# Optimization experiments

Hardware: AMD Instinct MI355X
Metric: run time of the kernel (lower is better)

The kernel has to match this reference:

```python
import jax, jax.numpy as jnp
import numpy as np

B, S, H = 32, 256, 1024   # batch, seq_len, xlmr hidden
HL = 512                  # lstm hidden per direction
E = 256                   # entity_feature_size
L = 5                     # languages: en fr de es it
LN_EPS = 1e-5


def setup_inputs() -> dict:
    key = jax.random.key(0)
    ks = jax.random.split(key, 12)
    sc = 0.02
    sequence_output = jax.random.normal(ks[0], (B, S, H), jnp.float32)
    lengths = jax.random.randint(ks[1], (B,), S // 2, S + 1)
    attention_mask = (jnp.arange(S)[None, :] < lengths[:, None]).astype(jnp.int32)
    language_ids = jax.random.randint(ks[2], (B,), 0, L).astype(jnp.int64)
    # per-language adapter params (stacked over lang dim)
    W1 = jax.random.normal(ks[3], (L, H, H), jnp.float32) * sc
    b1 = jnp.zeros((L, H), jnp.float32)
    ln_g = jnp.ones((L, H), jnp.float32)
    ln_b = jnp.zeros((L, H), jnp.float32)
    W2 = jax.random.normal(ks[4], (L, H, H), jnp.float32) * sc
    b2 = jnp.zeros((L, H), jnp.float32)
    # BiLSTM params, torch gate order (i, f, g, o); b = b_ih + b_hh
    Wih_f = jax.random.normal(ks[5], (4 * HL, H), jnp.float32) * sc
    Whh_f = jax.random.normal(ks[6], (4 * HL, HL), jnp.float32) * sc
    b_f = jnp.zeros((4 * HL,), jnp.float32)
    Wih_b = jax.random.normal(ks[7], (4 * HL, H), jnp.float32) * sc
    Whh_b = jax.random.normal(ks[8], (4 * HL, HL), jnp.float32) * sc
    b_b = jnp.zeros((4 * HL,), jnp.float32)
    # projection 2*HL -> E
    Wp = jax.random.normal(ks[9], (E, 2 * HL), jnp.float32) * sc
    bp = jnp.zeros((E,), jnp.float32)
    return dict(sequence_output=sequence_output, attention_mask=attention_mask,
                language_ids=language_ids, W1=W1, b1=b1, ln_g=ln_g, ln_b=ln_b,
                W2=W2, b2=b2, Wih_f=Wih_f, Whh_f=Whh_f, b_f=b_f,
                Wih_b=Wih_b, Whh_b=Whh_b, b_b=b_b, Wp=Wp, bp=bp)


def _lstm_scan(x, mask, Wih, Whh, b):
    """x: [S,B,H], mask: [S,B,1] bool. Returns hidden states [S,B,HL].
    Masked steps keep state and emit 0 (pack/pad_packed semantics)."""
    h0 = jnp.zeros((x.shape[1], Whh.shape[1]), x.dtype)

    def step(carry, inp):
        h, c = carry
        x_t, m = inp
        gates = x_t @ Wih.T + h @ Whh.T + b
        i, f, g, o = jnp.split(gates, 4, axis=-1)
        c_new = jax.nn.sigmoid(f) * c + jax.nn.sigmoid(i) * jnp.tanh(g)
        h_new = jax.nn.sigmoid(o) * jnp.tanh(c_new)
        h = jnp.where(m, h_new, h)
        c = jnp.where(m, c_new, c)
        return (h, c), jnp.where(m, h_new, 0.0)

    _, ys = jax.lax.scan(step, (h0, h0), (x, mask))
    return ys


def reference(sequence_output, attention_mask, language_ids, W1, b1, ln_g, ln_b,
              W2, b2, Wih_f, Whh_f, b_f, Wih_b, Whh_b, b_b, Wp, bp):
    # --- all 5 language adapters on the full batch, then masked-sum ---
    h = jnp.einsum('bsh,lhd->lbsd', sequence_output, W1) + b1[:, None, None, :]
    mu = h.mean(-1, keepdims=True)
    var = h.var(-1, keepdims=True)
    h = (h - mu) * jax.lax.rsqrt(var + LN_EPS) * ln_g[:, None, None, :] + ln_b[:, None, None, :]
    h = jax.nn.relu(h)
    h = jnp.einsum('lbsd,ldh->lbsh', h, W2) + b2[:, None, None, :]
    onehot = jax.nn.one_hot(language_ids, L, dtype=h.dtype)          # [B,L]
    adapted = jnp.einsum('lbsh,bl->bsh', h, onehot)                  # [B,S,H]
    # --- BiLSTM over valid lengths (packed-sequence semantics) ---
    x = adapted.transpose(1, 0, 2)                                    # [S,B,H]
    m = attention_mask.astype(bool).T[:, :, None]                     # [S,B,1]
    ys_f = _lstm_scan(x, m, Wih_f, Whh_f, b_f)                        # [S,B,HL]
    ys_b = _lstm_scan(x[::-1], m[::-1], Wih_b, Whh_b, b_b)[::-1]      # [S,B,HL]
    lstm_out = jnp.concatenate([ys_f, ys_b], -1).transpose(1, 0, 2)   # [B,S,2HL]
    return lstm_out @ Wp.T + bp                                       # [B,S,E]
```

## Files before the change

### kernel.cpp

```cpp
#include <hip/hip_runtime.h>

typedef __bf16 bft;
typedef bft bf16x8 __attribute__((ext_vector_type(8)));
typedef bft bf16x4 __attribute__((ext_vector_type(4)));
typedef bft bf16x2 __attribute__((ext_vector_type(2)));
typedef float f32x4 __attribute__((ext_vector_type(4)));
typedef unsigned long long u64;
typedef unsigned int u32;
typedef u32 u32x4 __attribute__((ext_vector_type(4)));

#define LN_EPS 1e-5f


__device__ __forceinline__ float sigmoidf_(float x) {
    return 1.f / (1.f + __expf(-x));
}
__device__ __forceinline__ float tanhf_(float x) {
    float e = __expf(-2.f * fabsf(x));
    float t = (1.f - e) / (1.f + e);
    return copysignf(t, x);
}

__global__ void cvt_f32_bf16(const float* __restrict__ in, bft* __restrict__ out, int n4) {
    int i = blockIdx.x * blockDim.x + threadIdx.x;
    if (i < n4) {
        float4 v = ((const float4*)in)[i];
        bf16x4 o = { (bft)v.x, (bft)v.y, (bft)v.z, (bft)v.w };
        ((bf16x4*)out)[i] = o;
    }
}

__global__ void zero_u32(u32* __restrict__ p, int n) {
    int i = blockIdx.x * blockDim.x + threadIdx.x;
    if (i < n) p[i] = 0u;
}

__global__ __launch_bounds__(256) void cvt_permute_wih(
    const float* __restrict__ in, bft* __restrict__ out)
{
    int r = blockIdx.x;
    int src = (r & 3) * 512 + (r >> 2);
    int t = threadIdx.x;
    float4 v = ((const float4*)(in + (size_t)src * 1024))[t];
    bf16x4 o = { (bft)v.x, (bft)v.y, (bft)v.z, (bft)v.w };
    ((bf16x4*)(out + (size_t)r * 1024))[t] = o;
}

__global__ void permute_bias(const float* __restrict__ in, float* __restrict__ out) {
    int t = blockIdx.x * blockDim.x + threadIdx.x;
    if (t < 2048) out[t] = in[(t & 3) * 512 + (t >> 2)];
}

__global__ __launch_bounds__(256) void transpose_cvt_w(
    const float* __restrict__ W1, const float* __restrict__ W2,
    bft* __restrict__ W1t, bft* __restrict__ W2t)
{
    __shared__ float tile[32][33];
    int z = blockIdx.z;
    int l = z >> 1;
    const float* src = ((z & 1) ? W2 : W1) + ((size_t)l << 20);
    bft* dst = ((z & 1) ? W2t : W1t) + ((size_t)l << 20);
    int tx = threadIdx.x & 31, ty = threadIdx.x >> 5;
    int bx = blockIdx.x * 32, by = blockIdx.y * 32;
    for (int r = ty; r < 32; r += 8)
        tile[r][tx] = src[(size_t)(by + r) * 1024 + bx + tx];
    __syncthreads();
    for (int r = ty; r < 32; r += 8)
        dst[(size_t)(bx + r) * 1024 + by + tx] = (bft)tile[tx][r];
}

__global__ __launch_bounds__(256) void gemm_bt(
    const bft* __restrict__ A, const bft* __restrict__ Bt,
    const float* __restrict__ bias, const int* __restrict__ langs,
    int langStrideB, int langStrideBias,
    float* __restrict__ outF, bft* __restrict__ outB,
    int remapLog, int remapMul, int ldc)
{
    const int K = 1024;
    int tn = blockIdx.x, tm = blockIdx.y;
    int row0 = tm * 128, col0 = tn * 128;
    int lang = langs ? langs[row0 >> 8] : 0;
    const bft* Ap = A + (size_t)row0 * K;
    const bft* Bp = Bt + (size_t)lang * langStrideB + (size_t)col0 * K;
    const float* biasp = bias + (size_t)lang * langStrideBias + col0;

    __shared__ bft As[128 * 32];
    __shared__ bft Bs[128 * 32];

    int t = threadIdx.x;
    int lane = t & 63, wave = t >> 6;
    int wm = wave & 1, wn = wave >> 1;
    int lrow = lane & 15, quad = lane >> 4;

    f32x4 acc[4][4] = {};

    for (int k0 = 0; k0 < K; k0 += 32) {
        __syncthreads();
        for (int c = t; c < 512; c += 256) {
            int r = c >> 2, co = (c & 3) << 3;
            *(uint4*)(As + r * 32 + co) = *(const uint4*)(Ap + (size_t)r * K + k0 + co);
            *(uint4*)(Bs + r * 32 + co) = *(const uint4*)(Bp + (size_t)r * K + k0 + co);
        }
        __syncthreads();
        bf16x8 af[4], bfr[4];
#pragma unroll
        for (int i = 0; i < 4; ++i)
            af[i] = *(const bf16x8*)(As + (wm * 64 + i * 16 + lrow) * 32 + quad * 8);
#pragma unroll
        for (int j = 0; j < 4; ++j)
            bfr[j] = *(const bf16x8*)(Bs + (wn * 64 + j * 16 + lrow) * 32 + quad * 8);
#pragma unroll
        for (int i = 0; i < 4; ++i)
#pragma unroll
            for (int j = 0; j < 4; ++j)
                acc[i][j] = __builtin_amdgcn_mfma_f32_16x16x32_bf16(af[i], bfr[j], acc[i][j], 0, 0, 0);
    }

#pragma unroll
    for (int i = 0; i < 4; ++i) {
#pragma unroll
        for (int j = 0; j < 4; ++j) {
#pragma unroll
            for (int r = 0; r < 4; ++r) {
                int m = wm * 64 + i * 16 + quad * 4 + r;
                int n = wn * 64 + j * 16 + lrow;
                int grow = row0 + m;
                int orow = remapLog ? ((grow & ((1 << remapLog) - 1)) * remapMul + (grow >> remapLog))
                                    : grow;
                float v = acc[i][j][r] + biasp[n];
                size_t idx = (size_t)orow * ldc + col0 + n;
                if (outF) outF[idx] = v;
                else outB[idx] = (bft)v;
            }
        }
    }
}

__global__ __launch_bounds__(256) void ln_relu_kernel(
    const float* __restrict__ h1, bft* __restrict__ a2,
    const float* __restrict__ ln_g, const float* __restrict__ ln_b,
    const int* __restrict__ langs)
{
    int row = blockIdx.x;
    int lang = langs[row >> 8];
    const float* x = h1 + (size_t)row * 1024;
    int t = threadIdx.x;
    float4 v = ((const float4*)x)[t];
    float s = v.x + v.y + v.z + v.w;
    float ss = v.x * v.x + v.y * v.y + v.z * v.z + v.w * v.w;
#pragma unroll
    for (int off = 32; off > 0; off >>= 1) {
        s += __shfl_down(s, off, 64);
        ss += __shfl_down(ss, off, 64);
    }
    __shared__ float red[8];
    int wave = t >> 6, lane = t & 63;
    if (lane == 0) { red[wave] = s; red[4 + wave] = ss; }
    __syncthreads();
    float S = red[0] + red[1] + red[2] + red[3];
    float SS = red[4] + red[5] + red[6] + red[7];
    float mean = S * (1.f / 1024.f);
    float var = SS * (1.f / 1024.f) - mean * mean;
    float inv = rsqrtf(var + LN_EPS);
    float4 g = ((const float4*)(ln_g + (size_t)lang * 1024))[t];
    float4 b = ((const float4*)(ln_b + (size_t)lang * 1024))[t];
    float y0 = fmaxf(0.f, (v.x - mean) * inv * g.x + b.x);
    float y1 = fmaxf(0.f, (v.y - mean) * inv * g.y + b.y);
    float y2 = fmaxf(0.f, (v.z - mean) * inv * g.z + b.z);
    float y3 = fmaxf(0.f, (v.w - mean) * inv * g.w + b.w);
    bf16x4 o = { (bft)y0, (bft)y1, (bft)y2, (bft)y3 };
    ((bf16x4*)(a2 + (size_t)row * 1024))[t] = o;
}

__global__ __launch_bounds__(256) void bilstm_kernel(
    const bft* __restrict__ gin_f, const bft* __restrict__ gin_b,
    const bft* __restrict__ Whh_f, const bft* __restrict__ Whh_b,
    const int* __restrict__ mask, bft* __restrict__ ys,
    u32* __restrict__ hg, u32* __restrict__ flg)
{
    __shared__ u64 smem[4096];
    bft* hs  = (bft*)smem;
    u32* hsd = (u32*)smem;

    int blk = blockIdx.x;
    int dir = blk >> 6;
    int gslice = blk & 63;
    int jbase = gslice << 3;
    const bft* Whh = dir ? Whh_b : Whh_f;
    const bft* gin = dir ? gin_b : gin_f;

    int t = threadIdx.x;
    int lane = t & 63, wave = t >> 6;
    int wm = wave & 1, wn = wave >> 1;
    int lrow = lane & 15, quad = lane >> 4;

    bf16x8 wf[16];
    {
        int row32 = wm * 16 + lrow;
        int jl = row32 >> 2, g = row32 & 3;
        const bft* wp = Whh + (size_t)(g * 512 + jbase + jl) * 512 + quad * 8;
#pragma unroll
        for (int kk = 0; kk < 16; ++kk)
            wf[kk] = *(const bf16x8*)(wp + kk * 32);
    }

    int batch = wn * 16 + lrow;
    int jl_out = wm * 4 + quad;
    const int* mrow = mask + batch * 256;
    u32* ysU = (u32*)ys;
    int mloS = t >> 6, b16S = t & 63;

    float cs = 0.f, hp = 0.f;

    for (int it = 0; it < 256; ++it) {
        int tt = dir ? (255 - it) : it;

        bf16x4 gv = *(const bf16x4*)(gin + ((size_t)(tt * 32 + batch) * 2048
                                            + (size_t)(jbase + jl_out) * 4));
        int mk = mrow[tt];

        if (it == 0) {
#pragma unroll
            for (int i = 0; i < 16; ++i)
                smem[t + i * 256] = 0ull;
        } else {
            if (wave == 0) {
                const u32* fp = flg + dir * 64 + lane;
                for (;;) {
                    u32 f = __hip_atomic_load(fp, __ATOMIC_RELAXED, __HIP_MEMORY_SCOPE_AGENT);
                    if (__all(f >= (u32)it)) break;
                    __builtin_amdgcn_s_sleep(1);
                }
            }
            __syncthreads();
            const u32* hq = hg + (size_t)(dir * 2 + (it & 1)) * 8192;
            u32x4 r[8];
#pragma unroll
            for (int i = 0; i < 8; ++i)
                asm volatile("global_load_dwordx4 %0, %1, off sc0 sc1"
                             : "=v"(r[i]) : "v"(hq + i * 1024 + t * 4) : "memory");
            asm volatile("s_waitcnt vmcnt(0)" ::: "memory");
#pragma unroll
            for (int i = 0; i < 8; ++i) {
                int m = i * 4 + mloS;
                *(u32x4*)(hsd + m * 256 + ((b16S ^ (m & 7)) << 2)) = r[i];
            }
        }
        __syncthreads();

        f32x4 acc0 = {}, acc1 = {};
#pragma unroll
        for (int kk = 0; kk < 16; ++kk) {
            int b16 = kk * 4 + quad;
            bf16x8 b = *(const bf16x8*)(hs + batch * 512 + ((b16 ^ (batch & 7)) << 3));
            if (kk & 1) acc1 = __builtin_amdgcn_mfma_f32_16x16x32_bf16(wf[kk], b, acc1, 0, 0, 0);
            else        acc0 = __builtin_amdgcn_mfma_f32_16x16x32_bf16(wf[kk], b, acc0, 0, 0, 0);
        }
        f32x4 acc = acc0 + acc1;

        float xi = acc[0] + (float)gv[0];
        float xf = acc[1] + (float)gv[1];
        float xg = acc[2] + (float)gv[2];
        float xo = acc[3] + (float)gv[3];
        float cn = sigmoidf_(xf) * cs + sigmoidf_(xi) * tanhf_(xg);
        float hn = sigmoidf_(xo) * tanhf_(cn);
        if (mk) { cs = cn; hp = hn; }
        union { bft h; unsigned short u; } hc; hc.h = (bft)hp;
        u32 own = (u32)hc.u | ((mk ? (u32)hc.u : 0u) << 16);
        u32 par = __shfl_xor(own, 16, 64);
        u32 hpair = (own & 0xffffu) | (par << 16);
        u32 ypair = (own >> 16) | (par & 0xffff0000u);

        if (!(lane & 16)) {
            u32* ha = hg + (size_t)(dir * 2 + ((it + 1) & 1)) * 8192
                         + batch * 256 + (jbase >> 1) + wm * 2 + (quad >> 1);
            asm volatile("global_store_dword %0, %1, off sc0 sc1" :: "v"(ha), "v"(hpair) : "memory");
        }
        asm volatile("s_waitcnt vmcnt(0)" ::: "memory");
        __syncthreads();
        if (t == 0 && it < 255)
            __hip_atomic_store(flg + dir * 64 + gslice, (u32)(it + 1),
                               __ATOMIC_RELAXED, __HIP_MEMORY_SCOPE_AGENT);
        if (!(lane & 16))
            ysU[((size_t)tt * 32 + batch) * 512 + dir * 256
                + (jbase >> 1) + wm * 2 + (quad >> 1)] = ypair;
    }
}

extern "C" void kernel_launch(void* const* d_in, const int* in_sizes, int n_in,
                              void* d_out, int out_size, void* d_ws, size_t ws_size,
                              hipStream_t stream)
{
    const float* X     = (const float*)d_in[0];
    const int*   amask = (const int*)d_in[1];
    const int*   langs = (const int*)d_in[2];
    const float* W1    = (const float*)d_in[3];
    const float* b1    = (const float*)d_in[4];
    const float* ln_g  = (const float*)d_in[5];
    const float* ln_b  = (const float*)d_in[6];
    const float* W2    = (const float*)d_in[7];
    const float* b2    = (const float*)d_in[8];
    const float* Wih_f = (const float*)d_in[9];
    const float* Whh_f = (const float*)d_in[10];
    const float* b_f   = (const float*)d_in[11];
    const float* Wih_b = (const float*)d_in[12];
    const float* Whh_b = (const float*)d_in[13];
    const float* b_b   = (const float*)d_in[14];
    const float* Wp    = (const float*)d_in[15];
    const float* bp    = (const float*)d_in[16];
    float* out = (float*)d_out;

    char* ws = (char*)d_ws;
    size_t off = 0;
    auto alloc = [&](size_t bytes) -> void* {
        void* p = ws + off;
        off += (bytes + 255) & ~(size_t)255;
        return p;
    };
    bft* Xbf   = (bft*)alloc(8192ull * 1024 * 2);
    bft* W1t   = (bft*)alloc(5ull * 1024 * 1024 * 2);
    bft* W2t   = (bft*)alloc(5ull * 1024 * 1024 * 2);
    bft* Wihf  = (bft*)alloc(2048ull * 1024 * 2);
    bft* Wihb  = (bft*)alloc(2048ull * 1024 * 2);
    bft* Whhf  = (bft*)alloc(2048ull * 512 * 2);
    bft* Whhb  = (bft*)alloc(2048ull * 512 * 2);
    bft* Wpb   = (bft*)alloc(256ull * 1024 * 2);
    float* h1  = (float*)alloc(8192ull * 1024 * 4);
    bft* a2    = (bft*)alloc(8192ull * 1024 * 2);
    bft* adapt = (bft*)alloc(8192ull * 1024 * 2);
    bft* ginf  = (bft*)alloc(256ull * 32 * 2048 * 2);
    bft* ginb  = (bft*)alloc(256ull * 32 * 2048 * 2);
    bft* ysb   = (bft*)alloc(256ull * 32 * 1024 * 2);
    float* pbf = (float*)alloc(2048ull * 4);
    float* pbb = (float*)alloc(2048ull * 4);
    u32* hg    = (u32*)alloc(2ull * 2 * 32 * 256 * 4);
    u32* flg   = (u32*)alloc(2ull * 64 * 4);
    (void)ws_size; (void)in_sizes; (void)n_in; (void)out_size;

    auto cvt = [&](const float* src, bft* dst, int n) {
        int n4 = n >> 2;
        hipLaunchKernelGGL(cvt_f32_bf16, dim3((n4 + 255) / 256), dim3(256), 0, stream, src, dst, n4);
    };
    cvt(X, Xbf, 8192 * 1024);
    hipLaunchKernelGGL(cvt_permute_wih, dim3(2048), dim3(256), 0, stream, Wih_f, Wihf);
    hipLaunchKernelGGL(cvt_permute_wih, dim3(2048), dim3(256), 0, stream, Wih_b, Wihb);
    cvt(Whh_f, Whhf, 2048 * 512);
    cvt(Whh_b, Whhb, 2048 * 512);
    cvt(Wp, Wpb, 256 * 1024);
    hipLaunchKernelGGL(permute_bias, dim3(8), dim3(256), 0, stream, b_f, pbf);
    hipLaunchKernelGGL(permute_bias, dim3(8), dim3(256), 0, stream, b_b, pbb);
    hipLaunchKernelGGL(zero_u32, dim3(1), dim3(256), 0, stream, flg, 128);
    hipLaunchKernelGGL(transpose_cvt_w, dim3(32, 32, 10), dim3(256), 0, stream, W1, W2, W1t, W2t);

    hipLaunchKernelGGL(gemm_bt, dim3(8, 64), dim3(256), 0, stream,
        Xbf, W1t, b1, langs, 1024 * 1024, 1024, h1, (bft*)nullptr, 0, 0, 1024);
    hipLaunchKernelGGL(ln_relu_kernel, dim3(8192), dim3(256), 0, stream, h1, a2, ln_g, ln_b, langs);
    hipLaunchKernelGGL(gemm_bt, dim3(8, 64), dim3(256), 0, stream,
        a2, W2t, b2, langs, 1024 * 1024, 1024, (float*)nullptr, adapt, 0, 0, 1024);
    hipLaunchKernelGGL(gemm_bt, dim3(16, 64), dim3(256), 0, stream,
        adapt, Wihf, pbf, (const int*)nullptr, 0, 0, (float*)nullptr, ginf, 8, 32, 2048);
    hipLaunchKernelGGL(gemm_bt, dim3(16, 64), dim3(256), 0, stream,
        adapt, Wihb, pbb, (const int*)nullptr, 0, 0, (float*)nullptr, ginb, 8, 32, 2048);
    {
        void* args[] = { (void*)&ginf, (void*)&ginb, (void*)&Whhf, (void*)&Whhb,
                         (void*)&amask, (void*)&ysb, (void*)&hg, (void*)&flg };
        hipLaunchCooperativeKernel((const void*)bilstm_kernel, dim3(128), dim3(256), args, 0, stream);
    }
    hipLaunchKernelGGL(gemm_bt, dim3(2, 64), dim3(256), 0, stream,
        ysb, Wpb, bp, (const int*)nullptr, 0, 0, out, (bft*)nullptr, 5, 256, 256);
}
```

Before: 1.326 ms.

## Use per-step arrival counters and coalesced gate/hidden layouts in BiLSTM

Replaces the per-block step flags in the persistent BiLSTM kernel with per-timestep atomic arrival counters, padded so each sits on its own cache line. Each wave increments its counter right after its own store, so the block-wide barrier before signalling is dropped. The input-gate GEMM now writes its output in a layout each LSTM thread can read contiguously, and the hidden-state exchange buffer is reorganised to match. The attention mask is pre-packed into bitwords so it is read once every 32 steps. The cost is a large counter array zeroed by an extra kernel, plus more complex index arithmetic in the GEMM epilogue.

```diff
diff --git a/kernel.cpp b/kernel.cpp
--- a/kernel.cpp
+++ b/kernel.cpp
@@ -33,6 +33,17 @@
 __global__ void zero_u32(u32* __restrict__ p, int n) {
     int i = blockIdx.x * blockDim.x + threadIdx.x;
     if (i < n) p[i] = 0u;
+}
+
+__global__ void pack_mask(const int* __restrict__ mask, u32* __restrict__ mbits) {
+    int t = blockIdx.x * blockDim.x + threadIdx.x;
+    if (t < 256) {
+        int w = t >> 5, b = t & 31;
+        u32 v = 0;
+        for (int i = 0; i < 32; ++i)
+            v |= (mask[b * 256 + w * 32 + i] ? 1u : 0u) << i;
+        mbits[w * 32 + b] = v;
+    }
 }
 
 __global__ __launch_bounds__(256) void cvt_permute_wih(
@@ -125,10 +136,20 @@
                 int m = wm * 64 + i * 16 + quad * 4 + r;
                 int n = wn * 64 + j * 16 + lrow;
                 int grow = row0 + m;
-                int orow = remapLog ? ((grow & ((1 << remapLog) - 1)) * remapMul + (grow >> remapLog))
-                                    : grow;
                 float v = acc[i][j][r] + biasp[n];
-                size_t idx = (size_t)orow * ldc + col0 + n;
+                size_t idx;
+                if (remapLog < 0) {
+                    int b = grow >> 8, s = grow & 255;
+                    int col = col0 + n;
+                    int jj = col >> 2, gg = col & 3;
+                    int jp = jj & 7, gs = jj >> 3;
+                    int tc = (((b >> 4) * 2 + (jp >> 2)) << 6) + ((jp & 3) << 4) + (b & 15);
+                    idx = (((size_t)s * 64 + gs) << 10) + (tc << 2) + gg;
+                } else {
+                    int orow = remapLog ? ((grow & ((1 << remapLog) - 1)) * remapMul + (grow >> remapLog))
+                                        : grow;
+                    idx = (size_t)orow * ldc + col0 + n;
+                }
                 if (outF) outF[idx] = v;
                 else outB[idx] = (bft)v;
             }
@@ -175,8 +196,8 @@
 __global__ __launch_bounds__(256) void bilstm_kernel(
     const bft* __restrict__ gin_f, const bft* __restrict__ gin_b,
     const bft* __restrict__ Whh_f, const bft* __restrict__ Whh_b,
-    const int* __restrict__ mask, bft* __restrict__ ys,
-    u32* __restrict__ hg, u32* __restrict__ flg)
+    const u32* __restrict__ mbits, bft* __restrict__ ys,
+    u32* __restrict__ hg, u32* __restrict__ ctr)
 {
     __shared__ u64 smem[4096];
     bft* hs  = (bft*)smem;
@@ -205,19 +226,16 @@
     }
 
     int batch = wn * 16 + lrow;
-    int jl_out = wm * 4 + quad;
-    const int* mrow = mask + batch * 256;
     u32* ysU = (u32*)ys;
-    int mloS = t >> 6, b16S = t & 63;
-
     float cs = 0.f, hp = 0.f;
+    u32 mw = 0;
 
     for (int it = 0; it < 256; ++it) {
         int tt = dir ? (255 - it) : it;
 
-        bf16x4 gv = *(const bf16x4*)(gin + ((size_t)(tt * 32 + batch) * 2048
-                                            + (size_t)(jbase + jl_out) * 4));
-        int mk = mrow[tt];
+        bf16x4 gv = *(const bf16x4*)(gin + ((((size_t)tt * 64 + gslice) << 10) + (t << 2)));
+        if ((it & 31) == 0) mw = mbits[(tt >> 5) * 32 + batch];
+        int mk = (mw >> (tt & 31)) & 1;
 
         if (it == 0) {
 #pragma unroll
@@ -225,10 +243,12 @@
                 smem[t + i * 256] = 0ull;
         } else {
             if (wave == 0) {
-                const u32* fp = flg + dir * 64 + lane;
+                u32 c = 8u;
+                const u32* cp = ctr + ((size_t)(dir * 256 + it) * 32 + (lane & 31)) * 16;
                 for (;;) {
-                    u32 f = __hip_atomic_load(fp, __ATOMIC_RELAXED, __HIP_MEMORY_SCOPE_AGENT);
-                    if (__all(f >= (u32)it)) break;
+                    if (lane < 32)
+                        c = __hip_atomic_load(cp, __ATOMIC_RELAXED, __HIP_MEMORY_SCOPE_AGENT);
+                    if (__all(c >= 8u)) break;
                     __builtin_amdgcn_s_sleep(1);
                 }
             }
@@ -242,8 +262,8 @@
             asm volatile("s_waitcnt vmcnt(0)" ::: "memory");
 #pragma unroll
             for (int i = 0; i < 8; ++i) {
-                int m = i * 4 + mloS;
-                *(u32x4*)(hsd + m * 256 + ((b16S ^ (m & 7)) << 2)) = r[i];
+                int bat = t & 31, gs = i * 8 + (t >> 5);
+                *(u32x4*)(hsd + bat * 256 + ((gs ^ (bat & 7)) << 2)) = r[i];
             }
         }
         __syncthreads();
@@ -273,14 +293,14 @@
 
         if (!(lane & 16)) {
             u32* ha = hg + (size_t)(dir * 2 + ((it + 1) & 1)) * 8192
-                         + batch * 256 + (jbase >> 1) + wm * 2 + (quad >> 1);
+                         + gslice * 128 + batch * 4 + wm * 2 + (quad >> 1);
             asm volatile("global_store_dword %0, %1, off sc0 sc1" :: "v"(ha), "v"(hpair) : "memory");
         }
         asm volatile("s_waitcnt vmcnt(0)" ::: "memory");
-        __syncthreads();
-        if (t == 0 && it < 255)
-            __hip_atomic_store(flg + dir * 64 + gslice, (u32)(it + 1),
-                               __ATOMIC_RELAXED, __HIP_MEMORY_SCOPE_AGENT);
+        if (lane == 0 && it < 255)
+            __hip_atomic_fetch_add(ctr + ((size_t)(dir * 256 + it + 1) * 32
+                                          + (gslice & 7) * 4 + wave) * 16,
+                                   1u, __ATOMIC_RELAXED, __HIP_MEMORY_SCOPE_AGENT);
         if (!(lane & 16))
             ysU[((size_t)tt * 32 + batch) * 512 + dir * 256
                 + (jbase >> 1) + wm * 2 + (quad >> 1)] = ypair;
@@ -333,8 +353,9 @@
     bft* ysb   = (bft*)alloc(256ull * 32 * 1024 * 2);
     float* pbf = (float*)alloc(2048ull * 4);
     float* pbb = (float*)alloc(2048ull * 4);
-    u32* hg    = (u32*)alloc(2ull * 2 * 32 * 256 * 4);
-    u32* flg   = (u32*)alloc(2ull * 64 * 4);
+    u32* hg    = (u32*)alloc(2ull * 2 * 64 * 32 * 4 * 4);
+    u32* ctr   = (u32*)alloc(2ull * 256 * 32 * 16 * 4);
+    u32* mbits = (u32*)alloc(256ull * 4);
     (void)ws_size; (void)in_sizes; (void)n_in; (void)out_size;
 
     auto cvt = [&](const float* src, bft* dst, int n) {
@@ -349,7 +370,8 @@
     cvt(Wp, Wpb, 256 * 1024);
     hipLaunchKernelGGL(permute_bias, dim3(8), dim3(256), 0, stream, b_f, pbf);
     hipLaunchKernelGGL(permute_bias, dim3(8), dim3(256), 0, stream, b_b, pbb);
-    hipLaunchKernelGGL(zero_u32, dim3(1), dim3(256), 0, stream, flg, 128);
+    hipLaunchKernelGGL(zero_u32, dim3(1024), dim3(256), 0, stream, ctr, 262144);
+    hipLaunchKernelGGL(pack_mask, dim3(1), dim3(256), 0, stream, amask, mbits);
     hipLaunchKernelGGL(transpose_cvt_w, dim3(32, 32, 10), dim3(256), 0, stream, W1, W2, W1t, W2t);
 
     hipLaunchKernelGGL(gemm_bt, dim3(8, 64), dim3(256), 0, stream,
@@ -358,12 +380,12 @@
     hipLaunchKernelGGL(gemm_bt, dim3(8, 64), dim3(256), 0, stream,
         a2, W2t, b2, langs, 1024 * 1024, 1024, (float*)nullptr, adapt, 0, 0, 1024);
     hipLaunchKernelGGL(gemm_bt, dim3(16, 64), dim3(256), 0, stream,
-        adapt, Wihf, pbf, (const int*)nullptr, 0, 0, (float*)nullptr, ginf, 8, 32, 2048);
+        adapt, Wihf, pbf, (const int*)nullptr, 0, 0, (float*)nullptr, ginf, -1, 0, 0);
     hipLaunchKernelGGL(gemm_bt, dim3(16, 64), dim3(256), 0, stream,
-        adapt, Wihb, pbb, (const int*)nullptr, 0, 0, (float*)nullptr, ginb, 8, 32, 2048);
+        adapt, Wihb, pbb, (const int*)nullptr, 0, 0, (float*)nullptr, ginb, -1, 0, 0);
     {
         void* args[] = { (void*)&ginf, (void*)&ginb, (void*)&Whhf, (void*)&Whhb,
-                         (void*)&amask, (void*)&ysb, (void*)&hg, (void*)&flg };
+                         (void*)&mbits, (void*)&ysb, (void*)&hg, (void*)&ctr };
         hipLaunchCooperativeKernel((const void*)bilstm_kernel, dim3(128), dim3(256), args, 0, stream);
     }
     hipLaunchKernelGGL(gemm_bt, dim3(2, 64), dim3(256), 0, stream,
```

Result: no change. 1.305 ms (-1.6%).
